# Kernel optimization log

Measured on AMD Instinct MI355X. Metric: run time of the kernel, lower is better.

The kernel has to match this reference:

```python
import jax, jax.numpy as jnp
import numpy as np

N_NODES = 100000
EMB_DIM = 128
HIDDEN = 64
N_EDGES = 1600000


def setup_inputs() -> dict:
    key = jax.random.key(0)
    k_emb, k_ei, k_w1, k_b1, k_w2, k_b2 = jax.random.split(key, 6)
    node_embeddings = jax.random.normal(k_emb, (N_NODES, EMB_DIM), dtype=jnp.float32)
    edge_index = jax.random.randint(k_ei, (2, N_EDGES), 0, N_NODES, dtype=jnp.int64)
    in_dim = 2 * EMB_DIM
    # Kaiming-uniform-ish init like torch Linear
    lim1 = 1.0 / np.sqrt(in_dim)
    lim2 = 1.0 / np.sqrt(HIDDEN)
    W1 = jax.random.uniform(k_w1, (in_dim, HIDDEN), minval=-lim1, maxval=lim1, dtype=jnp.float32)
    b1 = jax.random.uniform(k_b1, (HIDDEN,), minval=-lim1, maxval=lim1, dtype=jnp.float32)
    W2 = jax.random.uniform(k_w2, (HIDDEN, 1), minval=-lim2, maxval=lim2, dtype=jnp.float32)
    b2 = jax.random.uniform(k_b2, (1,), minval=-lim2, maxval=lim2, dtype=jnp.float32)
    return {"node_embeddings": node_embeddings, "edge_index": edge_index,
            "W1": W1, "b1": b1, "W2": W2, "b2": b2}


def reference(node_embeddings, edge_index, W1, b1, W2, b2):
    # Gather source/target node embeddings per edge
    src = node_embeddings[edge_index[0]]            # [E, D]
    tgt = node_embeddings[edge_index[1]]            # [E, D]
    edge_features = jnp.concatenate([src, tgt], axis=1)  # [E, 2D]
    h = jax.nn.relu(edge_features @ W1 + b1)        # [E, H]; dropout = identity (eval)
    edge_scores = (h @ W2 + b2).squeeze(-1)         # [E]
    return edge_scores
```

## Files before the change

kernel.cpp:

```cpp
#include <hip/hip_runtime.h>
#include <hip/hip_bf16.h>

typedef float f32x4 __attribute__((ext_vector_type(4)));
typedef __bf16 bf16x8 __attribute__((ext_vector_type(8)));
typedef _Float16 f16x2 __attribute__((ext_vector_type(2)));
typedef _Float16 f16x4 __attribute__((ext_vector_type(4)));
typedef _Float16 f16x8 __attribute__((ext_vector_type(8)));
typedef unsigned short u16;

__device__ inline u16 f2bf(float f) {
    unsigned int u = __float_as_uint(f);
    return (u16)((u + 0x7fffu + ((u >> 16) & 1u)) >> 16);
}

__device__ inline f16x2 pkrtz(float a, float b) {
    union { __fp16 h __attribute__((ext_vector_type(2))); f16x2 f; } r;
    r.h = __builtin_amdgcn_cvt_pkrtz(a, b);
    return r.f;
}

__global__ __launch_bounds__(256) void cvt_w_kernel(const float* __restrict__ W1,
                                                    u16* __restrict__ wf) {
    int i = blockIdx.x * 256 + threadIdx.x;
    if (i >= 128 * 128) return;
    int j = i & 7, fl = i >> 3;
    int lane = fl & 63, kbt = fl >> 6;
    int kb = kbt >> 3, t = kbt & 7;
    int k = kb * 32 + ((lane >> 4) & 3) * 8 + j;
    int n = t * 16 + (lane & 15);
    int krow = k + ((n >= 64) ? 128 : 0);
    wf[i] = f2bf(W1[krow * 64 + (n & 63)]);
}

__device__ inline bf16x8 pack8(const float4 a, const float4 b) {
    union { unsigned int w[4]; bf16x8 v; } r;
    asm("v_cvt_pk_bf16_f32 %0, %1, %2" : "=v"(r.w[0]) : "v"(a.x), "v"(a.y));
    asm("v_cvt_pk_bf16_f32 %0, %1, %2" : "=v"(r.w[1]) : "v"(a.z), "v"(a.w));
    asm("v_cvt_pk_bf16_f32 %0, %1, %2" : "=v"(r.w[2]) : "v"(b.x), "v"(b.y));
    asm("v_cvt_pk_bf16_f32 %0, %1, %2" : "=v"(r.w[3]) : "v"(b.z), "v"(b.w));
    return r.v;
}

__global__ __launch_bounds__(256) void uv_gemm_kernel(
    const float* __restrict__ emb, const u16* __restrict__ wf,
    const float* __restrict__ b1, _Float16* __restrict__ uv, int M) {
    __shared__ __align__(16) u16 bsh[32 * 64 * 8];

    const int tid = threadIdx.x;
    const int w = tid >> 6, lane = tid & 63, quad = lane >> 4, l15 = lane & 15;
    {
        const uint4* s = (const uint4*)wf;
        uint4* d = (uint4*)bsh;
#pragma unroll
        for (int i = 0; i < 8; ++i) d[tid + i * 256] = s[tid + i * 256];
    }
    __syncthreads();

    const int rb = blockIdx.x * 128 + w * 32;

    bf16x8 a[2][4];
#pragma unroll
    for (int m = 0; m < 2; ++m) {
        int row = rb + m * 16 + l15;
        if (row >= M) row = M - 1;
        const float* p = emb + (long)row * 128 + quad * 8;
#pragma unroll
        for (int kb = 0; kb < 4; ++kb) {
            float4 x = ((const float4*)(p + kb * 32))[0];
            float4 y = ((const float4*)(p + kb * 32))[1];
            a[m][kb] = pack8(x, y);
        }
    }

    f32x4 acc[2][8];
#pragma unroll
    for (int m = 0; m < 2; ++m)
#pragma unroll
        for (int t = 0; t < 8; ++t)
#pragma unroll
            for (int r = 0; r < 4; ++r) acc[m][t][r] = 0.0f;

#pragma unroll
    for (int kb = 0; kb < 4; ++kb)
#pragma unroll
        for (int t = 0; t < 8; ++t) {
            bf16x8 bf = *(const bf16x8*)(bsh + ((kb * 8 + t) * 64 + lane) * 8);
#pragma unroll
            for (int m = 0; m < 2; ++m)
                acc[m][t] = __builtin_amdgcn_mfma_f32_16x16x32_bf16(a[m][kb], bf,
                                                                    acc[m][t], 0, 0, 0);
        }

    float b1c[4];
#pragma unroll
    for (int t = 0; t < 4; ++t) b1c[t] = b1[t * 16 + l15];

#pragma unroll
    for (int m = 0; m < 2; ++m)
#pragma unroll
        for (int r = 0; r < 4; ++r) {
            int node = rb + m * 16 + quad * 4 + r;
            if (node >= M) continue;
            f16x2 u0 = pkrtz(acc[m][0][r] + b1c[0], acc[m][1][r] + b1c[1]);
            f16x2 u1 = pkrtz(acc[m][2][r] + b1c[2], acc[m][3][r] + b1c[3]);
            f16x2 v0 = pkrtz(acc[m][4][r], acc[m][5][r]);
            f16x2 v1 = pkrtz(acc[m][6][r], acc[m][7][r]);
            f16x4 su, sv;
            su[0] = u0[0]; su[1] = u0[1]; su[2] = u1[0]; su[3] = u1[1];
            sv[0] = v0[0]; sv[1] = v0[1]; sv[2] = v1[0]; sv[3] = v1[1];
            _Float16* p = uv + (long)node * 128 + l15 * 4;
            *(f16x4*)p = su;
            *(f16x4*)(p + 64) = sv;
        }
}

__device__ inline f16x2 relu2(f16x2 x) {
    f16x2 r;
    r[0] = (x[0] > (_Float16)0.f) ? x[0] : (_Float16)0.f;
    r[1] = (x[1] > (_Float16)0.f) ? x[1] : (_Float16)0.f;
    return r;
}

__device__ inline float dot2(f16x2 h, f16x2 w, float s) {
#if __has_builtin(__builtin_amdgcn_fdot2)
    return __builtin_amdgcn_fdot2(h, w, s, false);
#else
    return s + (float)h[0] * (float)w[0] + (float)h[1] * (float)w[1];
#endif
}

__global__ __launch_bounds__(256, 8) void edge_score_kernel(
    const _Float16* __restrict__ uv, const int* __restrict__ idx,
    const float* __restrict__ w2, const float* __restrict__ b2,
    float* __restrict__ out, int E, int nT) {
    const int tid = threadIdx.x, w = tid >> 6, lane = tid & 63;
    const int e4 = lane >> 2, q = lane & 3;

    f16x2 w2h[8];
#pragma unroll
    for (int i = 0; i < 8; ++i) {
        int s0 = 2 * i, s1 = 2 * i + 1;
        int d0 = ((s0 & 3) << 4) + (q << 2) + (s0 >> 2);
        int d1 = ((s1 & 3) << 4) + (q << 2) + (s1 >> 2);
        w2h[i][0] = (_Float16)w2[d0];
        w2h[i][1] = (_Float16)w2[d1];
    }
    const float b2v = b2[0];

    const int gw = blockIdx.x * 4 + w, stride = gridDim.x * 4;
    const int step = stride * 2;

    auto ldidx = [&](int tile, int& s, int& t) {
        int e = tile * 16 + e4;
        if (e >= E) e = E - 1;
        s = __builtin_nontemporal_load(idx + e);
        t = __builtin_nontemporal_load(idx + E + e);
    };

    union F8 { f16x8 v; f16x2 p[4]; };

    auto score16 = [&](int src, int tgt) -> float {
        const _Float16* up = uv + (long)src * 128 + q * 16;
        const _Float16* vp = uv + (long)tgt * 128 + 64 + q * 16;
        F8 U0, U1, V0, V1;
        U0.v = *(const f16x8*)up;
        U1.v = *(const f16x8*)(up + 8);
        V0.v = *(const f16x8*)vp;
        V1.v = *(const f16x8*)(vp + 8);
        float s = 0.f;
#pragma unroll
        for (int i = 0; i < 4; ++i) {
            f16x2 h = relu2(U0.p[i] + V0.p[i]);
            s = dot2(h, w2h[i], s);
        }
#pragma unroll
        for (int i = 0; i < 4; ++i) {
            f16x2 h = relu2(U1.p[i] + V1.p[i]);
            s = dot2(h, w2h[4 + i], s);
        }
        return s;
    };

    int sA, tA, sB, tB;
    {
        int t0 = (gw < nT) ? gw : 0;
        int t1 = (gw + stride < nT) ? (gw + stride) : t0;
        ldidx(t0, sA, tA);
        ldidx(t1, sB, tB);
    }

    for (int tile = gw; tile < nT; tile += step) {
        const int tileB = tile + stride;

        int n0 = tile + step, n1 = tile + step + stride;
        int sA2, tA2, sB2, tB2;
        ldidx(n0 < nT ? n0 : tile, sA2, tA2);
        ldidx(n1 < nT ? n1 : tile, sB2, tB2);

        float sa = score16(sA, tA);
        float sb = score16(sB, tB);

        sa += __shfl_xor(sa, 1, 64);
        sa += __shfl_xor(sa, 2, 64);
        sb += __shfl_xor(sb, 1, 64);
        sb += __shfl_xor(sb, 2, 64);

        if (q == 0) {
            int ea = tile * 16 + e4;
            if (ea < E) __builtin_nontemporal_store(sa + b2v, out + ea);
            if (tileB < nT) {
                int eb = tileB * 16 + e4;
                if (eb < E) __builtin_nontemporal_store(sb + b2v, out + eb);
            }
        }
        sA = sA2; tA = tA2; sB = sB2; tB = tB2;
    }
}

extern "C" void kernel_launch(void* const* d_in, const int* in_sizes, int n_in,
                              void* d_out, int out_size, void* d_ws, size_t ws_size,
                              hipStream_t stream) {
    const float* emb_f = (const float*)d_in[0];
    const int*   idx   = (const int*)d_in[1];
    const float* W1    = (const float*)d_in[2];
    const float* b1    = (const float*)d_in[3];
    const float* W2    = (const float*)d_in[4];
    const float* b2    = (const float*)d_in[5];
    float* out = (float*)d_out;

    const int embN = in_sizes[0];
    const int M    = embN / 128;
    const int E    = in_sizes[1] / 2;

    _Float16* uv = (_Float16*)d_ws;
    u16* wf = (u16*)(uv + (long)M * 128);

    cvt_w_kernel<<<64, 256, 0, stream>>>(W1, wf);
    uv_gemm_kernel<<<(M + 127) / 128, 256, 0, stream>>>(emb_f, wf, b1, uv, M);

    int nT = (E + 15) / 16;
    edge_score_kernel<<<2048, 256, 0, stream>>>(uv, idx, W2, b2, out, E, nT);
}
```

Before: 158.7 us.

## Quantize per-node U/V projections to int8 with per-row scales

The node projection tables U and V move from fp16 to int8, each node row carrying its own fp32 absmax scale computed with a cross-lane max reduction in the GEMM epilogue. This halves the bytes gathered per edge in the edge-scoring kernel, which is bound by random gathers. In exchange, dequantization moves into the edge loop as per-byte sign-extend, FMA and ReLU work in fp32, and the int8 quantization error may exceed the accuracy tolerance. Launch bounds on the edge kernel also drop from 8 to 4 waves.

```diff
diff --git a/kernel.cpp b/kernel.cpp
--- a/kernel.cpp
+++ b/kernel.cpp
@@ -3,20 +3,12 @@
 
 typedef float f32x4 __attribute__((ext_vector_type(4)));
 typedef __bf16 bf16x8 __attribute__((ext_vector_type(8)));
-typedef _Float16 f16x2 __attribute__((ext_vector_type(2)));
-typedef _Float16 f16x4 __attribute__((ext_vector_type(4)));
-typedef _Float16 f16x8 __attribute__((ext_vector_type(8)));
 typedef unsigned short u16;
+typedef unsigned char u8;
 
 __device__ inline u16 f2bf(float f) {
     unsigned int u = __float_as_uint(f);
     return (u16)((u + 0x7fffu + ((u >> 16) & 1u)) >> 16);
-}
-
-__device__ inline f16x2 pkrtz(float a, float b) {
-    union { __fp16 h __attribute__((ext_vector_type(2))); f16x2 f; } r;
-    r.h = __builtin_amdgcn_cvt_pkrtz(a, b);
-    return r.f;
 }
 
 __global__ __launch_bounds__(256) void cvt_w_kernel(const float* __restrict__ W1,
@@ -43,7 +35,8 @@
 
 __global__ __launch_bounds__(256) void uv_gemm_kernel(
     const float* __restrict__ emb, const u16* __restrict__ wf,
-    const float* __restrict__ b1, _Float16* __restrict__ uv, int M) {
+    const float* __restrict__ b1, u8* __restrict__ qu_tab, u8* __restrict__ qv_tab,
+    float* __restrict__ su_arr, float* __restrict__ sv_arr, int M) {
     __shared__ __align__(16) u16 bsh[32 * 64 * 8];
 
     const int tid = threadIdx.x;
@@ -100,51 +93,55 @@
 #pragma unroll
         for (int r = 0; r < 4; ++r) {
             int node = rb + m * 16 + quad * 4 + r;
-            if (node >= M) continue;
-            f16x2 u0 = pkrtz(acc[m][0][r] + b1c[0], acc[m][1][r] + b1c[1]);
-            f16x2 u1 = pkrtz(acc[m][2][r] + b1c[2], acc[m][3][r] + b1c[3]);
-            f16x2 v0 = pkrtz(acc[m][4][r], acc[m][5][r]);
-            f16x2 v1 = pkrtz(acc[m][6][r], acc[m][7][r]);
-            f16x4 su, sv;
-            su[0] = u0[0]; su[1] = u0[1]; su[2] = u1[0]; su[3] = u1[1];
-            sv[0] = v0[0]; sv[1] = v0[1]; sv[2] = v1[0]; sv[3] = v1[1];
-            _Float16* p = uv + (long)node * 128 + l15 * 4;
-            *(f16x4*)p = su;
-            *(f16x4*)(p + 64) = sv;
-        }
-}
-
-__device__ inline f16x2 relu2(f16x2 x) {
-    f16x2 r;
-    r[0] = (x[0] > (_Float16)0.f) ? x[0] : (_Float16)0.f;
-    r[1] = (x[1] > (_Float16)0.f) ? x[1] : (_Float16)0.f;
-    return r;
-}
-
-__device__ inline float dot2(f16x2 h, f16x2 w, float s) {
-#if __has_builtin(__builtin_amdgcn_fdot2)
-    return __builtin_amdgcn_fdot2(h, w, s, false);
-#else
-    return s + (float)h[0] * (float)w[0] + (float)h[1] * (float)w[1];
-#endif
-}
-
-__global__ __launch_bounds__(256, 8) void edge_score_kernel(
-    const _Float16* __restrict__ uv, const int* __restrict__ idx,
-    const float* __restrict__ w2, const float* __restrict__ b2,
-    float* __restrict__ out, int E, int nT) {
+            float uval[4], vval[4];
+#pragma unroll
+            for (int t = 0; t < 4; ++t) {
+                uval[t] = acc[m][t][r] + b1c[t];
+                vval[t] = acc[m][4 + t][r];
+            }
+            float au = fmaxf(fmaxf(fabsf(uval[0]), fabsf(uval[1])),
+                             fmaxf(fabsf(uval[2]), fabsf(uval[3])));
+            float av = fmaxf(fmaxf(fabsf(vval[0]), fabsf(vval[1])),
+                             fmaxf(fabsf(vval[2]), fabsf(vval[3])));
+#pragma unroll
+            for (int mk = 1; mk < 16; mk <<= 1) {
+                au = fmaxf(au, __shfl_xor(au, mk, 64));
+                av = fmaxf(av, __shfl_xor(av, mk, 64));
+            }
+            au = fmaxf(au, 1e-20f);
+            av = fmaxf(av, 1e-20f);
+            float iu = 127.0f / au, iv = 127.0f / av;
+            unsigned int ub = 0, vb = 0;
+#pragma unroll
+            for (int t = 0; t < 4; ++t) {
+                int qi = (int)rintf(uval[t] * iu);
+                int qj = (int)rintf(vval[t] * iv);
+                ub |= ((unsigned int)(qi & 255)) << (8 * t);
+                vb |= ((unsigned int)(qj & 255)) << (8 * t);
+            }
+            if (node < M) {
+                *(unsigned int*)(qu_tab + (long)node * 64 + l15 * 4) = ub;
+                *(unsigned int*)(qv_tab + (long)node * 64 + l15 * 4) = vb;
+                if (l15 == 0) {
+                    su_arr[node] = au * (1.0f / 127.0f);
+                    sv_arr[node] = av * (1.0f / 127.0f);
+                }
+            }
+        }
+}
+
+__global__ __launch_bounds__(256, 4) void edge_score_kernel(
+    const u8* __restrict__ qu_tab, const u8* __restrict__ qv_tab,
+    const float* __restrict__ su_arr, const float* __restrict__ sv_arr,
+    const int* __restrict__ idx, const float* __restrict__ w2,
+    const float* __restrict__ b2, float* __restrict__ out, int E, int nT) {
     const int tid = threadIdx.x, w = tid >> 6, lane = tid & 63;
     const int e4 = lane >> 2, q = lane & 3;
 
-    f16x2 w2h[8];
-#pragma unroll
-    for (int i = 0; i < 8; ++i) {
-        int s0 = 2 * i, s1 = 2 * i + 1;
-        int d0 = ((s0 & 3) << 4) + (q << 2) + (s0 >> 2);
-        int d1 = ((s1 & 3) << 4) + (q << 2) + (s1 >> 2);
-        w2h[i][0] = (_Float16)w2[d0];
-        w2h[i][1] = (_Float16)w2[d1];
-    }
+    float w2f[16];
+#pragma unroll
+    for (int s = 0; s < 16; ++s)
+        w2f[s] = w2[((s & 3) << 4) + (q << 2) + (s >> 2)];
     const float b2v = b2[0];
 
     const int gw = blockIdx.x * 4 + w, stride = gridDim.x * 4;
@@ -157,27 +154,24 @@
         t = __builtin_nontemporal_load(idx + E + e);
     };
 
-    union F8 { f16x8 v; f16x2 p[4]; };
-
     auto score16 = [&](int src, int tgt) -> float {
-        const _Float16* up = uv + (long)src * 128 + q * 16;
-        const _Float16* vp = uv + (long)tgt * 128 + 64 + q * 16;
-        F8 U0, U1, V0, V1;
-        U0.v = *(const f16x8*)up;
-        U1.v = *(const f16x8*)(up + 8);
-        V0.v = *(const f16x8*)vp;
-        V1.v = *(const f16x8*)(vp + 8);
+        const uint4 qu = *(const uint4*)(qu_tab + (long)src * 64 + q * 16);
+        const uint4 qv = *(const uint4*)(qv_tab + (long)tgt * 64 + q * 16);
+        const float su = su_arr[src];
+        const float sv = sv_arr[tgt];
+        const unsigned int ud[4] = {qu.x, qu.y, qu.z, qu.w};
+        const unsigned int vd[4] = {qv.x, qv.y, qv.z, qv.w};
         float s = 0.f;
 #pragma unroll
-        for (int i = 0; i < 4; ++i) {
-            f16x2 h = relu2(U0.p[i] + V0.p[i]);
-            s = dot2(h, w2h[i], s);
-        }
-#pragma unroll
-        for (int i = 0; i < 4; ++i) {
-            f16x2 h = relu2(U1.p[i] + V1.p[i]);
-            s = dot2(h, w2h[4 + i], s);
-        }
+        for (int k = 0; k < 4; ++k)
+#pragma unroll
+            for (int j = 0; j < 4; ++j) {
+                int a = ((int)(ud[k] << (24 - 8 * j))) >> 24;
+                int b = ((int)(vd[k] << (24 - 8 * j))) >> 24;
+                float h = fmaf((float)b, sv, (float)a * su);
+                h = fmaxf(h, 0.f);
+                s = fmaf(h, w2f[k * 4 + j], s);
+            }
         return s;
     };
 
@@ -232,12 +226,17 @@
     const int M    = embN / 128;
     const int E    = in_sizes[1] / 2;
 
-    _Float16* uv = (_Float16*)d_ws;
-    u16* wf = (u16*)(uv + (long)M * 128);
+    u8* qu = (u8*)d_ws;
+    u8* qv = qu + (long)M * 64;
+    float* su = (float*)(qv + (long)M * 64);
+    float* sv = su + M;
+    u16* wf = (u16*)(sv + M);
 
     cvt_w_kernel<<<64, 256, 0, stream>>>(W1, wf);
-    uv_gemm_kernel<<<(M + 127) / 128, 256, 0, stream>>>(emb_f, wf, b1, uv, M);
+    uv_gemm_kernel<<<(M + 127) / 128, 256, 0, stream>>>(emb_f, wf, b1, qu, qv,
+                                                        su, sv, M);
 
     int nT = (E + 15) / 16;
-    edge_score_kernel<<<2048, 256, 0, stream>>>(uv, idx, W2, b2, out, E, nT);
-}
+    edge_score_kernel<<<2048, 256, 0, stream>>>(qu, qv, su, sv, idx, W2, b2,
+                                                out, E, nT);
+}
```

Measured after the change: 163.4 us. +2.9%, slower.

## Bucket edges by source node range to improve gather locality

Applied to the files above, without the earlier changes.

Adds a scatter pass that splits edges into 8 buckets by source-node range, packing src, tgt and edge id into 64-bit entries. The scoring kernel then walks each bucket, with blocks assigned round-robin across buckets, so concurrent source gathers come from a narrower slice of the uv table and should hit L2/MALL more often. Target loads become nontemporal. The cost is an extra pass that reads the indices and writes 8 bytes per edge, plus atomics and scattered output stores; bucket capacity is fixed at E/8+65536, which assumes a roughly uniform source distribution.

```diff
diff --git a/kernel.cpp b/kernel.cpp
--- a/kernel.cpp
+++ b/kernel.cpp
@@ -7,6 +7,8 @@
 typedef _Float16 f16x4 __attribute__((ext_vector_type(4)));
 typedef _Float16 f16x8 __attribute__((ext_vector_type(8)));
 typedef unsigned short u16;
+typedef unsigned long long u64;
+typedef unsigned int u32;
 
 __device__ inline u16 f2bf(float f) {
     unsigned int u = __float_as_uint(f);
@@ -19,8 +21,19 @@
     return r.f;
 }
 
+__device__ inline bf16x8 pack8(const float4 a, const float4 b) {
+    union { unsigned int w[4]; bf16x8 v; } r;
+    asm("v_cvt_pk_bf16_f32 %0, %1, %2" : "=v"(r.w[0]) : "v"(a.x), "v"(a.y));
+    asm("v_cvt_pk_bf16_f32 %0, %1, %2" : "=v"(r.w[1]) : "v"(a.z), "v"(a.w));
+    asm("v_cvt_pk_bf16_f32 %0, %1, %2" : "=v"(r.w[2]) : "v"(b.x), "v"(b.y));
+    asm("v_cvt_pk_bf16_f32 %0, %1, %2" : "=v"(r.w[3]) : "v"(b.z), "v"(b.w));
+    return r.v;
+}
+
 __global__ __launch_bounds__(256) void cvt_w_kernel(const float* __restrict__ W1,
-                                                    u16* __restrict__ wf) {
+                                                    u16* __restrict__ wf,
+                                                    u32* __restrict__ cursors) {
+    if (blockIdx.x == 0 && threadIdx.x < 8) cursors[threadIdx.x] = 0;
     int i = blockIdx.x * 256 + threadIdx.x;
     if (i >= 128 * 128) return;
     int j = i & 7, fl = i >> 3;
@@ -30,15 +43,6 @@
     int n = t * 16 + (lane & 15);
     int krow = k + ((n >= 64) ? 128 : 0);
     wf[i] = f2bf(W1[krow * 64 + (n & 63)]);
-}
-
-__device__ inline bf16x8 pack8(const float4 a, const float4 b) {
-    union { unsigned int w[4]; bf16x8 v; } r;
-    asm("v_cvt_pk_bf16_f32 %0, %1, %2" : "=v"(r.w[0]) : "v"(a.x), "v"(a.y));
-    asm("v_cvt_pk_bf16_f32 %0, %1, %2" : "=v"(r.w[1]) : "v"(a.z), "v"(a.w));
-    asm("v_cvt_pk_bf16_f32 %0, %1, %2" : "=v"(r.w[2]) : "v"(b.x), "v"(b.y));
-    asm("v_cvt_pk_bf16_f32 %0, %1, %2" : "=v"(r.w[3]) : "v"(b.z), "v"(b.w));
-    return r.v;
 }
 
 __global__ __launch_bounds__(256) void uv_gemm_kernel(
@@ -114,6 +118,43 @@
         }
 }
 
+#define SCAT_EPT 4
+__global__ __launch_bounds__(256) void bucket_scatter_kernel(
+    const int* __restrict__ idx, u64* __restrict__ buckets,
+    u32* __restrict__ cursors, int E, int cap, int div) {
+    __shared__ u32 hist[8], base[8], lcur[8];
+    const int tid = threadIdx.x;
+    if (tid < 8) { hist[tid] = 0; lcur[tid] = 0; }
+    __syncthreads();
+
+    const int e0 = blockIdx.x * (256 * SCAT_EPT) + tid;
+    int myb[SCAT_EPT], mys[SCAT_EPT], myt[SCAT_EPT];
+#pragma unroll
+    for (int k = 0; k < SCAT_EPT; ++k) {
+        int e = e0 + k * 256;
+        myb[k] = -1;
+        if (e < E) {
+            mys[k] = idx[e];
+            myt[k] = idx[E + e];
+            myb[k] = mys[k] / div;
+            atomicAdd(&hist[myb[k]], 1u);
+        }
+    }
+    __syncthreads();
+    if (tid < 8) base[tid] = atomicAdd(&cursors[tid], hist[tid]);
+    __syncthreads();
+#pragma unroll
+    for (int k = 0; k < SCAT_EPT; ++k) {
+        int b = myb[k];
+        if (b >= 0) {
+            u32 off = atomicAdd(&lcur[b], 1u);
+            int e = e0 + k * 256;
+            u64 ent = (u64)(u32)mys[k] | ((u64)(u32)myt[k] << 17) | ((u64)(u32)e << 34);
+            buckets[(long)b * cap + base[b] + off] = ent;
+        }
+    }
+}
+
 __device__ inline f16x2 relu2(f16x2 x) {
     f16x2 r;
     r[0] = (x[0] > (_Float16)0.f) ? x[0] : (_Float16)0.f;
@@ -129,44 +170,37 @@
 #endif
 }
 
-__global__ __launch_bounds__(256, 8) void edge_score_kernel(
-    const _Float16* __restrict__ uv, const int* __restrict__ idx,
-    const float* __restrict__ w2, const float* __restrict__ b2,
-    float* __restrict__ out, int E, int nT) {
+__global__ __launch_bounds__(256, 8) void edge_score_bucketed(
+    const _Float16* __restrict__ uv, const u64* __restrict__ buckets,
+    const u32* __restrict__ cursors, const float* __restrict__ w2,
+    const float* __restrict__ b2, float* __restrict__ out, int cap) {
     const int tid = threadIdx.x, w = tid >> 6, lane = tid & 63;
     const int e4 = lane >> 2, q = lane & 3;
 
+    const int b = blockIdx.x & 7;
+    const int blkin = blockIdx.x >> 3;
+    const int cnt = (int)cursors[b];
+    if (cnt <= 0) return;
+    const u64* bk = buckets + (long)b * cap;
+
     f16x2 w2h[8];
 #pragma unroll
     for (int i = 0; i < 8; ++i) {
         int s0 = 2 * i, s1 = 2 * i + 1;
-        int d0 = ((s0 & 3) << 4) + (q << 2) + (s0 >> 2);
-        int d1 = ((s1 & 3) << 4) + (q << 2) + (s1 >> 2);
-        w2h[i][0] = (_Float16)w2[d0];
-        w2h[i][1] = (_Float16)w2[d1];
+        w2h[i][0] = (_Float16)w2[((s0 & 3) << 4) + (q << 2) + (s0 >> 2)];
+        w2h[i][1] = (_Float16)w2[((s1 & 3) << 4) + (q << 2) + (s1 >> 2)];
     }
     const float b2v = b2[0];
 
-    const int gw = blockIdx.x * 4 + w, stride = gridDim.x * 4;
-    const int step = stride * 2;
-
-    auto ldidx = [&](int tile, int& s, int& t) {
-        int e = tile * 16 + e4;
-        if (e >= E) e = E - 1;
-        s = __builtin_nontemporal_load(idx + e);
-        t = __builtin_nontemporal_load(idx + E + e);
-    };
-
     union F8 { f16x8 v; f16x2 p[4]; };
-
     auto score16 = [&](int src, int tgt) -> float {
         const _Float16* up = uv + (long)src * 128 + q * 16;
         const _Float16* vp = uv + (long)tgt * 128 + 64 + q * 16;
         F8 U0, U1, V0, V1;
         U0.v = *(const f16x8*)up;
         U1.v = *(const f16x8*)(up + 8);
-        V0.v = *(const f16x8*)vp;
-        V1.v = *(const f16x8*)(vp + 8);
+        V0.v = __builtin_nontemporal_load((const f16x8*)vp);
+        V1.v = __builtin_nontemporal_load((const f16x8*)vp + 1);
         float s = 0.f;
 #pragma unroll
         for (int i = 0; i < 4; ++i) {
@@ -181,24 +215,20 @@
         return s;
     };
 
-    int sA, tA, sB, tB;
-    {
-        int t0 = (gw < nT) ? gw : 0;
-        int t1 = (gw + stride < nT) ? (gw + stride) : t0;
-        ldidx(t0, sA, tA);
-        ldidx(t1, sB, tB);
-    }
-
-    for (int tile = gw; tile < nT; tile += step) {
-        const int tileB = tile + stride;
-
-        int n0 = tile + step, n1 = tile + step + stride;
-        int sA2, tA2, sB2, tB2;
-        ldidx(n0 < nT ? n0 : tile, sA2, tA2);
-        ldidx(n1 < nT ? n1 : tile, sB2, tB2);
-
-        float sa = score16(sA, tA);
-        float sb = score16(sB, tB);
+    const int wavein = blkin * 4 + w;
+    const int stepA = 1024 * 16;
+    for (int p0 = wavein * 16; p0 < cnt; p0 += 2 * stepA) {
+        const int posA = p0 + e4;
+        const int posB = p0 + stepA + e4;
+        const bool actA = posA < cnt, actB = posB < cnt;
+        u64 entA = __builtin_nontemporal_load(bk + (actA ? posA : 0));
+        u64 entB = __builtin_nontemporal_load(bk + (actB ? posB : 0));
+
+        int srcA = (int)(entA & 0x1FFFF), tgtA = (int)((entA >> 17) & 0x1FFFF);
+        int srcB = (int)(entB & 0x1FFFF), tgtB = (int)((entB >> 17) & 0x1FFFF);
+
+        float sa = score16(srcA, tgtA);
+        float sb = actB ? score16(srcB, tgtB) : 0.f;
 
         sa += __shfl_xor(sa, 1, 64);
         sa += __shfl_xor(sa, 2, 64);
@@ -206,14 +236,9 @@
         sb += __shfl_xor(sb, 2, 64);
 
         if (q == 0) {
-            int ea = tile * 16 + e4;
-            if (ea < E) __builtin_nontemporal_store(sa + b2v, out + ea);
-            if (tileB < nT) {
-                int eb = tileB * 16 + e4;
-                if (eb < E) __builtin_nontemporal_store(sb + b2v, out + eb);
-            }
-        }
-        sA = sA2; tA = tA2; sB = sB2; tB = tB2;
+            if (actA) __builtin_nontemporal_store(sa + b2v, out + (int)(entA >> 34));
+            if (actB) __builtin_nontemporal_store(sb + b2v, out + (int)(entB >> 34));
+        }
     }
 }
 
@@ -234,10 +259,17 @@
 
     _Float16* uv = (_Float16*)d_ws;
     u16* wf = (u16*)(uv + (long)M * 128);
-
-    cvt_w_kernel<<<64, 256, 0, stream>>>(W1, wf);
+    u32* cursors = (u32*)(wf + 128 * 128);
+    u64* buckets = (u64*)((char*)cursors + 256);
+
+    const int div = (M + 7) / 8;
+    const int cap = E / 8 + 65536;
+
+    cvt_w_kernel<<<64, 256, 0, stream>>>(W1, wf, cursors);
     uv_gemm_kernel<<<(M + 127) / 128, 256, 0, stream>>>(emb_f, wf, b1, uv, M);
 
-    int nT = (E + 15) / 16;
-    edge_score_kernel<<<2048, 256, 0, stream>>>(uv, idx, W2, b2, out, E, nT);
-}
+    const int nscat = (E + 256 * SCAT_EPT - 1) / (256 * SCAT_EPT);
+    bucket_scatter_kernel<<<nscat, 256, 0, stream>>>(idx, buckets, cursors, E, cap, div);
+
+    edge_score_bucketed<<<2048, 256, 0, stream>>>(uv, buckets, cursors, W2, b2, out, cap);
+}
```

New measurement: 202.9 us. 27.8% more time.
